# Optimization experiments

Measured on AMD Instinct MI355X. Metric: run time of the kernel, lower is better.

Reference implementation:

```python
import jax, jax.numpy as jnp
import numpy as np

B, N, DIM = 2, 2048, 1024
NUM_HEADS = 16
EFF = NUM_HEADS // 2          # 8 effective heads
HD = DIM // NUM_HEADS         # 64
LAMBDA_INIT = 0.8
EPS = 1e-5


def setup_inputs() -> dict:
    key = jax.random.key(0)
    ks = jax.random.split(key, 16)
    s = 0.02
    return {
        "x":  jax.random.normal(ks[0], (B, N, DIM), dtype=jnp.float32),
        "Wq": jax.random.normal(ks[1], (DIM, DIM), dtype=jnp.float32) * s,
        "bq": jnp.zeros((DIM,), dtype=jnp.float32),
        "Wk": jax.random.normal(ks[2], (DIM, DIM), dtype=jnp.float32) * s,
        "bk": jnp.zeros((DIM,), dtype=jnp.float32),
        "Wv": jax.random.normal(ks[3], (DIM, DIM), dtype=jnp.float32) * s,
        "bv": jnp.zeros((DIM,), dtype=jnp.float32),
        "Wo": jax.random.normal(ks[4], (DIM, DIM), dtype=jnp.float32) * s,
        "bo": jnp.zeros((DIM,), dtype=jnp.float32),
        "norm_w": jnp.ones((2 * HD,), dtype=jnp.float32),
        "lq1": jax.random.normal(ks[5], (HD,), dtype=jnp.float32) * 0.1,
        "lk1": jax.random.normal(ks[6], (HD,), dtype=jnp.float32) * 0.1,
        "lq2": jax.random.normal(ks[7], (HD,), dtype=jnp.float32) * 0.1,
        "lk2": jax.random.normal(ks[8], (HD,), dtype=jnp.float32) * 0.1,
    }


def reference(x, Wq, bq, Wk, bk, Wv, bv, Wo, bo, norm_w, lq1, lk1, lq2, lk2):
    scale = HD ** -0.5
    # projections (torch Linear: y = x @ W.T + b)
    q = (x @ Wq.T + bq).reshape(B, N, NUM_HEADS, HD).transpose(0, 2, 1, 3) * scale  # [B,2E,N,hd]
    k = (x @ Wk.T + bk).reshape(B, N, NUM_HEADS, HD).transpose(0, 2, 1, 3)          # [B,2E,N,hd]
    v = (x @ Wv.T + bv).reshape(B, N, EFF, 2 * HD).transpose(0, 2, 1, 3)            # [B,E,N,2hd]

    scores = jnp.einsum('bhqd,bhkd->bhqk', q, k)              # [B,2E,N,N]
    probs = jax.nn.softmax(scores, axis=-1)
    probs = probs.reshape(B, EFF, 2, N, N)                    # pair consecutive heads

    lam = jnp.exp(jnp.sum(lq1 * lk1)) - jnp.exp(jnp.sum(lq2 * lk2)) + LAMBDA_INIT
    diff = probs[:, :, 0] - lam * probs[:, :, 1]              # [B,E,N,N]

    out = jnp.einsum('behk,bekd->behd'.replace('e','h').replace('hh','h') if False else 'bhqk,bhkd->bhqd', diff, v)  # [B,E,N,2hd]
    # headwise RMSNorm over last dim (2*hd)
    out = out * jax.lax.rsqrt(jnp.mean(out * out, axis=-1, keepdims=True) + EPS) * norm_w
    out = out * (1.0 - LAMBDA_INIT)

    out = out.transpose(0, 2, 1, 3).reshape(B, N, DIM)
    return out @ Wo.T + bo
```

## Files before the change

kernel.cpp:

```cpp
#include <hip/hip_runtime.h>
#include <hip/hip_bf16.h>

#define B_   2
#define N_   2048
#define DIM_ 1024
#define HD_  64
#define DV_  128

typedef __bf16 bf16;
typedef __bf16 bf16x8 __attribute__((ext_vector_type(8)));
typedef __bf16 bf16x4 __attribute__((ext_vector_type(4)));
typedef float  floatx4 __attribute__((ext_vector_type(4)));
typedef float  floatx16 __attribute__((ext_vector_type(16)));
typedef unsigned int uint;
typedef uint uint2v __attribute__((ext_vector_type(2)));
typedef uint uint4v __attribute__((ext_vector_type(4)));

#if __has_builtin(__builtin_amdgcn_exp2f)
#define EXP2(x) __builtin_amdgcn_exp2f(x)
#else
#define EXP2(x) exp2f(x)
#endif

#define QSCALE 0.1803368801111244f

__device__ __forceinline__ void async16(const void* g, void* l) {
  __builtin_amdgcn_global_load_lds(
      (__attribute__((address_space(1))) void*)g,
      (__attribute__((address_space(3))) void*)l, 16, 0, 0);
}

__device__ __forceinline__ uint packbf(float a, float b) {
  unsigned short ul = __builtin_bit_cast(unsigned short, (bf16)a);
  unsigned short uh = __builtin_bit_cast(unsigned short, (bf16)b);
  return (uint)ul | ((uint)uh << 16);
}

__global__ void convert_kernel(const float* __restrict__ x,
                               const float* __restrict__ wq,
                               const float* __restrict__ wk,
                               const float* __restrict__ wv,
                               const float* __restrict__ wo,
                               bf16* __restrict__ dst) {
  const int NX = B_ * N_ * DIM_;
  const int NW = DIM_ * DIM_;
  int i = (blockIdx.x * 256 + threadIdx.x) * 4;
  const float* src;
  int off;
  if (i < NX) { src = x; off = i; }
  else {
    int j = i - NX;
    int w = j >> 20;
    off = j & (NW - 1);
    src = (w == 0) ? wq : (w == 1) ? wk : (w == 2) ? wv : wo;
  }
  float4 v = *(const float4*)(src + off);
  bf16x4 o = { (bf16)v.x, (bf16)v.y, (bf16)v.z, (bf16)v.w };
  *(bf16x4*)(dst + i) = o;
}

__global__ __launch_bounds__(256) void proj_kernel(
    const bf16* __restrict__ xb, const bf16* __restrict__ wall,
    const float* __restrict__ bq, const float* __restrict__ bk,
    const float* __restrict__ bv,
    bf16* __restrict__ qo, bf16* __restrict__ ko, bf16* __restrict__ vt) {
  __shared__ __align__(16) bf16 SM[2 * 128 * 64];
  bf16* At = SM;
  bf16* Bt = SM + 128 * 64;
  const int tid = threadIdx.x, lane = tid & 63, w = tid >> 6;
  const int tm = blockIdx.x, tn = blockIdx.y, z = blockIdx.z;
  const int quad = lane >> 4, l15 = lane & 15;
  const int wm = (w >> 1) * 64, wn = (w & 1) * 64;
  const bf16* Ab = xb + (long)tm * 128 * DIM_;
  const bf16* Bb = wall + (long)z * (DIM_ * DIM_) + (long)tn * 128 * DIM_;
  floatx4 zero = {0.f, 0.f, 0.f, 0.f};
  floatx4 acc[4][4];
#pragma unroll
  for (int i = 0; i < 4; ++i)
#pragma unroll
    for (int j = 0; j < 4; ++j) acc[i][j] = zero;

  for (int kb = 0; kb < DIM_ / 64; ++kb) {
    for (int idx = tid; idx < 1024; idx += 256) {
      int row = idx >> 3, ch = idx & 7, g = ch ^ (row & 7);
      async16(Ab + row * DIM_ + kb * 64 + g * 8, (char*)At + (idx - lane) * 16);
      async16(Bb + row * DIM_ + kb * 64 + g * 8, (char*)Bt + (idx - lane) * 16);
    }
    __syncthreads();
#pragma unroll
    for (int ks = 0; ks < 2; ++ks) {
      bf16x8 af[4], bfm[4];
#pragma unroll
      for (int mt = 0; mt < 4; ++mt) {
        int r = wm + mt * 16 + l15;
        af[mt] = *(const bf16x8*)&At[r * 64 + ((ks * 4 + quad) ^ (r & 7)) * 8];
      }
#pragma unroll
      for (int nt = 0; nt < 4; ++nt) {
        int r = wn + nt * 16 + l15;
        bfm[nt] = *(const bf16x8*)&Bt[r * 64 + ((ks * 4 + quad) ^ (r & 7)) * 8];
      }
#pragma unroll
      for (int mt = 0; mt < 4; ++mt)
#pragma unroll
        for (int nt = 0; nt < 4; ++nt)
          acc[mt][nt] = __builtin_amdgcn_mfma_f32_16x16x32_bf16(
              af[mt], bfm[nt], acc[mt][nt], 0, 0, 0);
    }
    __syncthreads();
  }

  if (z != 2) {
#pragma unroll
    for (int mt = 0; mt < 4; ++mt)
#pragma unroll
      for (int nt = 0; nt < 4; ++nt)
#pragma unroll
        for (int r = 0; r < 4; ++r) {
          int grow = tm * 128 + wm + mt * 16 + quad * 4 + r;
          int gcol = tn * 128 + wn + nt * 16 + l15;
          float v = acc[mt][nt][r];
          if (z == 0) {
            qo[(long)grow * DIM_ + gcol] = (bf16)((v + bq[gcol]) * QSCALE);
          } else {
            ko[(long)grow * DIM_ + gcol] = (bf16)(v + bk[gcol]);
          }
        }
  } else {
    bf16* Vl = SM;
#pragma unroll
    for (int nt = 0; nt < 4; ++nt) {
      int d = wn + nt * 16 + l15;
      float bvv = bv[tn * 128 + d];
      int m = (d & 7) * 2;
#pragma unroll
      for (int mt = 0; mt < 4; ++mt) {
        bf16x4 v4 = { (bf16)(acc[mt][nt][0] + bvv), (bf16)(acc[mt][nt][1] + bvv),
                      (bf16)(acc[mt][nt][2] + bvv), (bf16)(acc[mt][nt][3] + bvv) };
        int c = (wm >> 2) + mt * 4 + quad;
        *(bf16x4*)&Vl[d * 128 + (c ^ m) * 4] = v4;
      }
    }
    __syncthreads();
    const int bb = tm >> 4, e = tn;
    const long rowbase = ((long)(bb * 8 + e) * 128) * (long)N_ + (tm & 15) * 128;
#pragma unroll
    for (int p = 0; p < 8; ++p) {
      int d = p * 16 + (tid >> 4), j = tid & 15;
      int cs = (2 * j) ^ ((d & 7) * 2);
      bf16x8 val = *(const bf16x8*)&Vl[d * 128 + cs * 4];
      *(bf16x8*)&vt[rowbase + (long)d * N_ + j * 8] = val;
    }
  }
}

__global__ __launch_bounds__(512, 2) void attn_kernel(
    const bf16* __restrict__ qb, const bf16* __restrict__ kbuf,
    const bf16* __restrict__ vt,
    const float* __restrict__ lq1, const float* __restrict__ lk1,
    const float* __restrict__ lq2, const float* __restrict__ lk2,
    const float* __restrict__ norm_w, bf16* __restrict__ ao) {
  __shared__ __align__(16) char smem[65536];

  const int tid = threadIdx.x, lane = tid & 63, w = tid >> 6;
  const int qt = blockIdx.x, e = blockIdx.y, b = blockIdx.z;
  const int hl = w & 1, qh = w >> 1;
  const int h = lane >> 5, l31 = lane & 31;
  const int qbase = qt * 128;

  bf16x8 qf[4];
  {
    const bf16* qrp = qb + (long)(b * N_ + qbase + qh * 32 + l31) * DIM_
                      + e * 128 + hl * 64 + h * 8;
#pragma unroll
    for (int c = 0; c < 4; ++c) qf[c] = *(const bf16x8*)(qrp + c * 16);
  }

  const bf16* kbase = kbuf + (long)b * N_ * DIM_ + e * 128;
  const bf16* vbase = vt + (long)(b * 8 + e) * DV_ * N_;

  floatx16 acc[4];
#pragma unroll
  for (int dt = 0; dt < 4; ++dt) acc[dt] = floatx16{};
  float lp = 0.f;

#define STAGE(ktv, bufv)                                                            \
  {                                                                                 \
    int kt_ = (ktv);                                                                \
    char* kdst = smem + (bufv) * 16384;                                             \
    char* vdst = smem + 32768 + (bufv) * 16384;                                     \
    _Pragma("unroll") for (int t = 0; t < 2; ++t) {                                 \
      int idx = tid + t * 512;                                                      \
      int khl = idx >> 9, row = (idx >> 3) & 63, ch = idx & 7;                      \
      int g = ch ^ (row & 7) ^ ((row >> 3) & 3);                                    \
      async16(kbase + ((long)(kt_ * 64 + row)) * DIM_ + khl * 64 + g * 8,           \
              kdst + (idx - lane) * 16);                                            \
    }                                                                               \
    _Pragma("unroll") for (int t = 0; t < 2; ++t) {                                 \
      int idx = tid + t * 512;                                                      \
      int row = idx >> 3, ch = idx & 7;                                             \
      int g = ch ^ (row & 7) ^ ((row >> 3) & 3);                                    \
      async16(vbase + (long)row * N_ + kt_ * 64 + g * 8,                            \
              vdst + (idx - lane) * 16);                                            \
    }                                                                               \
  }

  STAGE(0, 0);

  for (int kt = 0; kt < N_ / 64; ++kt) {
    const int buf = kt & 1;
    __syncthreads();
    if (kt + 1 < N_ / 64) STAGE(kt + 1, buf ^ 1);

    const bf16* Kh = (const bf16*)(smem + buf * 16384) + hl * 4096;
    const bf16* Vb = (const bf16*)(smem + 32768 + buf * 16384);

    bf16x8 kfrag[2][4], vfrag[4][4];
#pragma unroll
    for (int kt2 = 0; kt2 < 2; ++kt2)
#pragma unroll
      for (int c = 0; c < 4; ++c) {
        int row = kt2 * 32 + l31;
        int sw = (c * 2 + h) ^ (row & 7) ^ ((row >> 3) & 3);
        kfrag[kt2][c] = *(const bf16x8*)&Kh[row * 64 + sw * 8];
      }
#pragma unroll
    for (int dt = 0; dt < 4; ++dt)
#pragma unroll
      for (int kc = 0; kc < 4; ++kc) {
        int row = dt * 32 + l31;
        int sw = (kc * 2 + h) ^ (row & 7) ^ ((row >> 3) & 3);
        vfrag[dt][kc] = *(const bf16x8*)&Vb[row * 64 + sw * 8];
      }

    bf16x8 af[2][2];
#pragma unroll
    for (int kt2 = 0; kt2 < 2; ++kt2) {
      floatx16 sv{};
#pragma unroll
      for (int c = 0; c < 4; ++c)
        sv = __builtin_amdgcn_mfma_f32_32x32x16_bf16(kfrag[kt2][c], qf[c], sv, 0, 0, 0);
      float t[16];
      float s = 0.f;
#pragma unroll
      for (int i = 0; i < 16; ++i) { t[i] = EXP2(sv[i]); s += t[i]; }
      lp += s;
      uint d0 = packbf(t[0], t[1]),   d1 = packbf(t[2], t[3]);
      uint d2 = packbf(t[4], t[5]),   d3 = packbf(t[6], t[7]);
      uint d4 = packbf(t[8], t[9]),   d5 = packbf(t[10], t[11]);
      uint d6 = packbf(t[12], t[13]), d7 = packbf(t[14], t[15]);
      uint4v f0, f1;
#if __has_builtin(__builtin_amdgcn_permlane32_swap)
      uint2v r02 = __builtin_amdgcn_permlane32_swap(d0, d2, false, false);
      uint2v r13 = __builtin_amdgcn_permlane32_swap(d1, d3, false, false);
      f0 = uint4v{r02.x, r13.x, r02.y, r13.y};
      uint2v r46 = __builtin_amdgcn_permlane32_swap(d4, d6, false, false);
      uint2v r57 = __builtin_amdgcn_permlane32_swap(d5, d7, false, false);
      f1 = uint4v{r46.x, r57.x, r46.y, r57.y};
#else
      uint e0 = __shfl_xor((int)d0, 32, 64), e1 = __shfl_xor((int)d1, 32, 64);
      uint e2 = __shfl_xor((int)d2, 32, 64), e3 = __shfl_xor((int)d3, 32, 64);
      uint e4 = __shfl_xor((int)d4, 32, 64), e5 = __shfl_xor((int)d5, 32, 64);
      uint e6 = __shfl_xor((int)d6, 32, 64), e7 = __shfl_xor((int)d7, 32, 64);
      f0 = h ? uint4v{e2, e3, d2, d3} : uint4v{d0, d1, e0, e1};
      f1 = h ? uint4v{e6, e7, d6, d7} : uint4v{d4, d5, e4, e5};
#endif
      af[kt2][0] = __builtin_bit_cast(bf16x8, f0);
      af[kt2][1] = __builtin_bit_cast(bf16x8, f1);
    }
#pragma unroll
    for (int dt = 0; dt < 4; ++dt)
#pragma unroll
      for (int kt2 = 0; kt2 < 2; ++kt2)
#pragma unroll
        for (int u = 0; u < 2; ++u)
          acc[dt] = __builtin_amdgcn_mfma_f32_32x32x16_bf16(
              af[kt2][u], vfrag[dt][kt2 * 2 + u], acc[dt], 0, 0, 0);
  }

  lp += __shfl_xor(lp, 32, 64);

  float* Ob = (float*)smem;
  __syncthreads();

  if (hl == 1) {
#pragma unroll
    for (int r = 0; r < 16; ++r) {
      int qloc = (r & 3) + 8 * (r >> 2) + 4 * h;
      float inv = 1.0f / __shfl(lp, qloc, 64);
      float* row = &Ob[(qh * 32 + qloc) * 128 + l31];
#pragma unroll
      for (int dt = 0; dt < 4; ++dt) row[dt * 32] = acc[dt][r] * inv;
    }
  }
  __syncthreads();
  if (hl == 0) {
    float la = lq1[lane] * lk1[lane];
    float lb = lq2[lane] * lk2[lane];
#pragma unroll
    for (int m = 1; m < 64; m <<= 1) {
      la += __shfl_xor(la, m, 64);
      lb += __shfl_xor(lb, m, 64);
    }
    float lam = __expf(la) - __expf(lb) + 0.8f;
    float nw4[4];
#pragma unroll
    for (int dt = 0; dt < 4; ++dt) nw4[dt] = norm_w[dt * 32 + l31] * 0.2f;
#pragma unroll
    for (int r = 0; r < 16; ++r) {
      int qloc = (r & 3) + 8 * (r >> 2) + 4 * h;
      float inv = 1.0f / __shfl(lp, qloc, 64);
      const float* row = &Ob[(qh * 32 + qloc) * 128 + l31];
      float v[4], ss = 0.f;
#pragma unroll
      for (int dt = 0; dt < 4; ++dt) {
        v[dt] = acc[dt][r] * inv - lam * row[dt * 32];
        ss += v[dt] * v[dt];
      }
#pragma unroll
      for (int msk = 1; msk < 32; msk <<= 1) ss += __shfl_xor(ss, msk, 64);
      float rms = rsqrtf(ss * (1.0f / 128.0f) + 1e-5f);
      int n = qbase + qh * 32 + qloc;
      bf16* dst = ao + (long)(b * N_ + n) * DIM_ + e * DV_ + l31;
#pragma unroll
      for (int dt = 0; dt < 4; ++dt) dst[dt * 32] = (bf16)(v[dt] * rms * nw4[dt]);
    }
  }
}

__global__ __launch_bounds__(512) void out_gemm(
    const bf16* __restrict__ ab, const bf16* __restrict__ wo,
    const float* __restrict__ bo, float* __restrict__ out) {
  __shared__ __align__(16) bf16 At[128 * 64];
  __shared__ __align__(16) bf16 Bt[128 * 64];
  const int tid = threadIdx.x, lane = tid & 63, w = tid >> 6;
  const int tm = blockIdx.x, tn = blockIdx.y;
  const int quad = lane >> 4, l15 = lane & 15;
  const int wm = (w & 3) * 32, wn = (w >> 2) * 64;
  const bf16* Ab = ab + (long)tm * 128 * DIM_;
  const bf16* Bb = wo + (long)tn * 128 * DIM_;
  floatx4 zero = {0.f, 0.f, 0.f, 0.f};
  floatx4 acc[2][4];
#pragma unroll
  for (int i = 0; i < 2; ++i)
#pragma unroll
    for (int j = 0; j < 4; ++j) acc[i][j] = zero;

  for (int kb = 0; kb < DIM_ / 64; ++kb) {
    for (int idx = tid; idx < 1024; idx += 512) {
      int row = idx >> 3, ch = idx & 7, g = ch ^ (row & 7);
      async16(Ab + row * DIM_ + kb * 64 + g * 8, (char*)At + (idx - lane) * 16);
      async16(Bb + row * DIM_ + kb * 64 + g * 8, (char*)Bt + (idx - lane) * 16);
    }
    __syncthreads();
#pragma unroll
    for (int ks = 0; ks < 2; ++ks) {
      bf16x8 af[2], bfm[4];
#pragma unroll
      for (int mt = 0; mt < 2; ++mt) {
        int r = wm + mt * 16 + l15;
        af[mt] = *(const bf16x8*)&At[r * 64 + ((ks * 4 + quad) ^ (r & 7)) * 8];
      }
#pragma unroll
      for (int nt = 0; nt < 4; ++nt) {
        int r = wn + nt * 16 + l15;
        bfm[nt] = *(const bf16x8*)&Bt[r * 64 + ((ks * 4 + quad) ^ (r & 7)) * 8];
      }
#pragma unroll
      for (int mt = 0; mt < 2; ++mt)
#pragma unroll
        for (int nt = 0; nt < 4; ++nt)
          acc[mt][nt] = __builtin_amdgcn_mfma_f32_16x16x32_bf16(
              af[mt], bfm[nt], acc[mt][nt], 0, 0, 0);
    }
    __syncthreads();
  }
#pragma unroll
  for (int mt = 0; mt < 2; ++mt)
#pragma unroll
    for (int nt = 0; nt < 4; ++nt)
#pragma unroll
      for (int r = 0; r < 4; ++r) {
        int grow = tm * 128 + wm + mt * 16 + quad * 4 + r;
        int gcol = tn * 128 + wn + nt * 16 + l15;
        out[(long)grow * DIM_ + gcol] = acc[mt][nt][r] + bo[gcol];
      }
}

extern "C" void kernel_launch(void* const* d_in, const int* in_sizes, int n_in,
                              void* d_out, int out_size, void* d_ws, size_t ws_size,
                              hipStream_t stream) {
  const float* x    = (const float*)d_in[0];
  const float* Wq   = (const float*)d_in[1];
  const float* bq   = (const float*)d_in[2];
  const float* Wk   = (const float*)d_in[3];
  const float* bk   = (const float*)d_in[4];
  const float* Wv   = (const float*)d_in[5];
  const float* bv   = (const float*)d_in[6];
  const float* Wo   = (const float*)d_in[7];
  const float* bo   = (const float*)d_in[8];
  const float* nw   = (const float*)d_in[9];
  const float* lq1  = (const float*)d_in[10];
  const float* lk1  = (const float*)d_in[11];
  const float* lq2  = (const float*)d_in[12];
  const float* lk2  = (const float*)d_in[13];

  char* ws = (char*)d_ws;
  bf16* xb   = (bf16*)(ws + 256);
  bf16* wqb  = xb + 4194304;
  bf16* qb   = wqb + 4 * 1048576;
  bf16* kbuf = qb + 4194304;
  bf16* vtb  = kbuf + 4194304;
  bf16* ab   = vtb + 4194304;

  convert_kernel<<<8192, 256, 0, stream>>>(x, Wq, Wk, Wv, Wo, xb);
  proj_kernel<<<dim3(32, 8, 3), 256, 0, stream>>>(xb, wqb, bq, bk, bv, qb, kbuf, vtb);
  attn_kernel<<<dim3(16, 8, 2), 512, 0, stream>>>(qb, kbuf, vtb, lq1, lk1, lq2, lk2,
                                                  nw, ab);
  out_gemm<<<dim3(32, 8), 512, 0, stream>>>(ab, wqb + 3 * 1048576, bo, (float*)d_out);
}
```

Measured before the change: 209.4 us.

## Double-buffer LDS tiles in projection and output GEMMs to overlap loads

```diff
diff --git a/kernel.cpp b/kernel.cpp
--- a/kernel.cpp
+++ b/kernel.cpp
@@ -64,9 +64,7 @@
     const float* __restrict__ bq, const float* __restrict__ bk,
     const float* __restrict__ bv,
     bf16* __restrict__ qo, bf16* __restrict__ ko, bf16* __restrict__ vt) {
-  __shared__ __align__(16) bf16 SM[2 * 128 * 64];
-  bf16* At = SM;
-  bf16* Bt = SM + 128 * 64;
+  __shared__ __align__(16) bf16 SM[2 * 16384];
   const int tid = threadIdx.x, lane = tid & 63, w = tid >> 6;
   const int tm = blockIdx.x, tn = blockIdx.y, z = blockIdx.z;
   const int quad = lane >> 4, l15 = lane & 15;
@@ -80,13 +78,25 @@
 #pragma unroll
     for (int j = 0; j < 4; ++j) acc[i][j] = zero;
 
+#define PSTAGE(kbv, bufv)                                                           \
+  {                                                                                 \
+    bf16* At_ = SM + (bufv) * 16384;                                                \
+    bf16* Bt_ = At_ + 8192;                                                         \
+    for (int idx = tid; idx < 1024; idx += 256) {                                   \
+      int row = idx >> 3, ch = idx & 7, g = ch ^ (row & 7);                         \
+      async16(Ab + row * DIM_ + (kbv) * 64 + g * 8, (char*)At_ + (idx - lane) * 16);\
+      async16(Bb + row * DIM_ + (kbv) * 64 + g * 8, (char*)Bt_ + (idx - lane) * 16);\
+    }                                                                               \
+  }
+
+  PSTAGE(0, 0);
+
   for (int kb = 0; kb < DIM_ / 64; ++kb) {
-    for (int idx = tid; idx < 1024; idx += 256) {
-      int row = idx >> 3, ch = idx & 7, g = ch ^ (row & 7);
-      async16(Ab + row * DIM_ + kb * 64 + g * 8, (char*)At + (idx - lane) * 16);
-      async16(Bb + row * DIM_ + kb * 64 + g * 8, (char*)Bt + (idx - lane) * 16);
-    }
+    const int buf = kb & 1;
     __syncthreads();
+    if (kb + 1 < DIM_ / 64) PSTAGE(kb + 1, buf ^ 1);
+    const bf16* At = SM + buf * 16384;
+    const bf16* Bt = At + 8192;
 #pragma unroll
     for (int ks = 0; ks < 2; ++ks) {
       bf16x8 af[4], bfm[4];
@@ -107,7 +117,6 @@
           acc[mt][nt] = __builtin_amdgcn_mfma_f32_16x16x32_bf16(
               af[mt], bfm[nt], acc[mt][nt], 0, 0, 0);
     }
-    __syncthreads();
   }
 
   if (z != 2) {
@@ -127,6 +136,7 @@
           }
         }
   } else {
+    __syncthreads();
     bf16* Vl = SM;
 #pragma unroll
     for (int nt = 0; nt < 4; ++nt) {
@@ -331,8 +341,7 @@
 __global__ __launch_bounds__(512) void out_gemm(
     const bf16* __restrict__ ab, const bf16* __restrict__ wo,
     const float* __restrict__ bo, float* __restrict__ out) {
-  __shared__ __align__(16) bf16 At[128 * 64];
-  __shared__ __align__(16) bf16 Bt[128 * 64];
+  __shared__ __align__(16) bf16 OS[2 * 16384];
   const int tid = threadIdx.x, lane = tid & 63, w = tid >> 6;
   const int tm = blockIdx.x, tn = blockIdx.y;
   const int quad = lane >> 4, l15 = lane & 15;
@@ -346,13 +355,25 @@
 #pragma unroll
     for (int j = 0; j < 4; ++j) acc[i][j] = zero;
 
+#define OSTAGE(kbv, bufv)                                                           \
+  {                                                                                 \
+    bf16* At_ = OS + (bufv) * 16384;                                                \
+    bf16* Bt_ = At_ + 8192;                                                         \
+    for (int idx = tid; idx < 1024; idx += 512) {                                   \
+      int row = idx >> 3, ch = idx & 7, g = ch ^ (row & 7);                         \
+      async16(Ab + row * DIM_ + (kbv) * 64 + g * 8, (char*)At_ + (idx - lane) * 16);\
+      async16(Bb + row * DIM_ + (kbv) * 64 + g * 8, (char*)Bt_ + (idx - lane) * 16);\
+    }                                                                               \
+  }
+
+  OSTAGE(0, 0);
+
   for (int kb = 0; kb < DIM_ / 64; ++kb) {
-    for (int idx = tid; idx < 1024; idx += 512) {
-      int row = idx >> 3, ch = idx & 7, g = ch ^ (row & 7);
-      async16(Ab + row * DIM_ + kb * 64 + g * 8, (char*)At + (idx - lane) * 16);
-      async16(Bb + row * DIM_ + kb * 64 + g * 8, (char*)Bt + (idx - lane) * 16);
-    }
+    const int buf = kb & 1;
     __syncthreads();
+    if (kb + 1 < DIM_ / 64) OSTAGE(kb + 1, buf ^ 1);
+    const bf16* At = OS + buf * 16384;
+    const bf16* Bt = At + 8192;
 #pragma unroll
     for (int ks = 0; ks < 2; ++ks) {
       bf16x8 af[2], bfm[4];
@@ -373,7 +394,6 @@
           acc[mt][nt] = __builtin_amdgcn_mfma_f32_16x16x32_bf16(
               af[mt], bfm[nt], acc[mt][nt], 0, 0, 0);
     }
-    __syncthreads();
   }
 #pragma unroll
   for (int mt = 0; mt < 2; ++mt)
```

Measured after the change: 211.7 us, median of 2. About the same (+1.1%).
